# Performance work log

Hardware: AMD Instinct MI355X
Metric: run time of the kernel (lower is better)

Reference implementation:

```python
import jax, jax.numpy as jnp
import numpy as np


def conv1x1(x, w, b):
    # 1x1 Conv2d: x [B,C,H,W], w [O,C], b [O] -> [B,O,H,W]
    return jnp.einsum('bchw,oc->bohw', x, w) + b[None, :, None, None]


def setup_inputs() -> dict:
    key = jax.random.key(0)
    ks = jax.random.split(key, 10)
    B, C, Ci, H, W = 4, 64, 32, 64, 64
    s = 0.05
    return {
        'supp_feature': jax.random.normal(ks[0], (B, C, H, W), jnp.float32),
        'ref_feature': jax.random.normal(ks[1], (B, C, H, W), jnp.float32),
        'theta_w': jax.random.normal(ks[2], (Ci, C), jnp.float32) * s,
        'theta_b': jax.random.normal(ks[3], (Ci,), jnp.float32) * s,
        'phi_w': jax.random.normal(ks[4], (Ci, C), jnp.float32) * s,
        'phi_b': jax.random.normal(ks[5], (Ci,), jnp.float32) * s,
        'g_w': jax.random.normal(ks[6], (Ci, C), jnp.float32) * s,
        'g_b': jax.random.normal(ks[7], (Ci,), jnp.float32) * s,
        'w_w': jax.random.normal(ks[8], (C, Ci), jnp.float32) * s,
        'w_b': jax.random.normal(ks[9], (C,), jnp.float32) * s,
    }


def reference(supp_feature, ref_feature, theta_w, theta_b, phi_w, phi_b,
              g_w, g_b, w_w, w_b):
    B, C, H, W = supp_feature.shape
    Ci = theta_w.shape[0]
    N = H * W
    theta_x = conv1x1(supp_feature, theta_w, theta_b).reshape(B, Ci, N)  # [B,Ci,N]
    phi_y = conv1x1(ref_feature, phi_w, phi_b).reshape(B, Ci, N)        # [B,Ci,M]
    g_y = conv1x1(ref_feature, g_w, g_b).reshape(B, Ci, N)              # [B,Ci,M]
    # f[b,n,m] = <theta_x[b,:,n], phi_y[b,:,m]>  (unscaled)
    f = jnp.einsum('bcn,bcm->bnm', theta_x, phi_y)
    # NOTE: softmax over dim=1 (the QUERY axis n), matching F.softmax(f, dim=1)
    f_div_C = jax.nn.softmax(f, axis=1)
    # x1[b,c,n] = sum_m f_div_C[b,n,m] * g_y[b,c,m]
    x1 = jnp.einsum('bnm,bcm->bcn', f_div_C, g_y).reshape(B, Ci, H, W)
    z = supp_feature + conv1x1(x1, w_w, w_b)
    return z
```

## Files before the change

### kernel.cpp

```cpp
#include <hip/hip_runtime.h>

#define C_ 64
#define CI_ 32
#define N_ 4096
#define LOG2E 1.4426950408889634f

typedef __attribute__((ext_vector_type(8))) short bf16x8;
typedef __attribute__((ext_vector_type(4))) float f32x4;

__device__ __forceinline__ unsigned short f2bf_rne(float f) {
  unsigned u = __builtin_bit_cast(unsigned, f);
  unsigned r = (u + 0x7FFFu + ((u >> 16) & 1u)) >> 16;
  return (unsigned short)r;
}
__device__ __forceinline__ unsigned pack_bf2(float lo, float hi) {
  unsigned a = (__builtin_bit_cast(unsigned, lo) + 0x8000u) >> 16;
  unsigned b = (__builtin_bit_cast(unsigned, hi) + 0x8000u) & 0xFFFF0000u;
  return a | b;
}
__device__ __forceinline__ void dma16(const void* gp, const void* lp) {
  __builtin_amdgcn_global_load_lds(
      (const __attribute__((address_space(1))) unsigned*)(unsigned long long)gp,
      (__attribute__((address_space(3))) unsigned*)(unsigned)(unsigned long long)lp,
      16, 0, 0);
}


__global__ __launch_bounds__(256) void k1_proj(
    const float* __restrict__ supp, const float* __restrict__ ref,
    const float* __restrict__ tw, const float* __restrict__ tb,
    const float* __restrict__ pw, const float* __restrict__ pb,
    const float* __restrict__ gw, const float* __restrict__ gb,
    unsigned short* __restrict__ theta, unsigned short* __restrict__ phi2,
    unsigned short* __restrict__ g2)
{
  const int proj = blockIdx.x >> 8;
  const int rr = blockIdx.x & 255;
  const int b = rr >> 6;
  const int n0 = (rr & 63) << 6;
  const int o = __builtin_amdgcn_readfirstlane(threadIdx.x >> 6);
  const int lane = threadIdx.x & 63;
  const int n = n0 + lane;

  __shared__ float gL[CI_][66];

  const float *W, *bias, *src;
  if (proj == 0)      { W = tw; bias = tb; src = supp; }
  else if (proj == 1) { W = pw; bias = pb; src = ref; }
  else                { W = gw; bias = gb; src = ref; }

  const float* x = src + (size_t)b * (C_ * N_) + n;
  const float* Wo = W + o * 8 * C_;
  float acc[8];
#pragma unroll
  for (int k = 0; k < 8; k++) acc[k] = bias[o * 8 + k];
#pragma unroll 8
  for (int c = 0; c < C_; c++) {
    float v = x[(size_t)c * N_];
#pragma unroll
    for (int k = 0; k < 8; k++) acc[k] = fmaf(Wo[k * C_ + c], v, acc[k]);
  }

  if (proj == 0) {
    unsigned pk[4];
#pragma unroll
    for (int k = 0; k < 4; k++)
      pk[k] = (unsigned)f2bf_rne(acc[2 * k] * LOG2E) |
              ((unsigned)f2bf_rne(acc[2 * k + 1] * LOG2E) << 16);
    *(uint4*)(theta + (((size_t)b * N_ + n) << 5) + o * 8) = *(uint4*)pk;
  } else if (proj == 1) {
    unsigned pk[4];
#pragma unroll
    for (int k = 0; k < 4; k++)
      pk[k] = (unsigned)f2bf_rne(acc[2 * k]) |
              ((unsigned)f2bf_rne(acc[2 * k + 1]) << 16);
    size_t off = (((size_t)b * 128 + (n >> 5)) << 10) + o * 256 + (n & 31) * 8;
    *(uint4*)(phi2 + off) = *(uint4*)pk;
  } else {
#pragma unroll
    for (int k = 0; k < 8; k++) gL[o * 8 + k][lane] = acc[k];
    __syncthreads();
    const int t = threadIdx.x;
    const int c = t >> 7;
    const int rr2 = t & 127;
    const int q = rr2 >> 5;
    const int i = rr2 & 31;
    const float* g0 = &gL[i][c * 32 + 4 * q];
    unsigned pk[4];
    pk[0] = pack_bf2(g0[0], g0[1]);
    pk[1] = pack_bf2(g0[2], g0[3]);
    pk[2] = pack_bf2(g0[16], g0[17]);
    pk[3] = pack_bf2(g0[18], g0[19]);
    size_t off = (((size_t)b * 128 + (n0 >> 5) + c) << 10) + rr2 * 8;
    *(uint4*)(g2 + off) = *(uint4*)pk;
  }
}

__global__ __launch_bounds__(256) void k2_den(
    const unsigned short* __restrict__ theta, const unsigned short* __restrict__ phi2,
    const float* __restrict__ ww, float* __restrict__ den,
    unsigned short* __restrict__ ww2)
{
  const int mt = blockIdx.x & 63;
  const int nq = (blockIdx.x >> 6) & 3;
  const int b = blockIdx.x >> 8;
  const int tid = threadIdx.x;
  const int w = tid >> 6;
  const int lane = tid & 63;
  const int row16 = lane & 15;
  const int quad = lane >> 4;

  if (blockIdx.x == 0) {
    for (int e = tid; e < C_ * CI_; e += 256) {
      int p = e & 31;
      int i = 4 * ((p >> 3) & 3) + (p & 3) + 16 * ((p >> 2) & 1);
      ww2[e] = f2bf_rne(ww[(e >> 5) * CI_ + i]);
    }
  }

  __shared__ __align__(16) unsigned short TH[2][2048];

  bf16x8 bf = *(const bf16x8*)(phi2 +
      (((size_t)b * 128 + mt * 2 + (w >> 1)) << 10) + (quad << 8) +
      ((w & 1) * 16 + row16) * 8);

  const unsigned short* thbase = theta + (((size_t)b * N_ + nq * 1024) << 5);

  dma16(thbase + w * 512 + lane * 8, &TH[0][w * 512]);
  __syncthreads();

  f32x4 zero = {0.f, 0.f, 0.f, 0.f};
  float ds4[4] = {0.f, 0.f, 0.f, 0.f};

  for (int ph = 0; ph < 16; ph++) {
    const int buf = ph & 1;
    if (ph + 1 < 16)
      dma16(thbase + (ph + 1) * 2048 + w * 512 + lane * 8, &TH[buf ^ 1][w * 512]);
#pragma unroll
    for (int s = 0; s < 4; s++) {
      bf16x8 af = *(const bf16x8*)(&TH[buf][s * 512 + row16 * 32 + quad * 8]);
      f32x4 ff = __builtin_amdgcn_mfma_f32_16x16x32_bf16(af, bf, zero, 0, 0, 0);
#pragma unroll
      for (int r = 0; r < 4; r++) ds4[r] += __builtin_amdgcn_exp2f(ff[r]);
    }
    __syncthreads();
  }

  float v = (ds4[0] + ds4[1]) + (ds4[2] + ds4[3]);
  v += __shfl_xor(v, 16);
  v += __shfl_xor(v, 32);
  if (lane < 16) {
    int ml64 = w * 16 + lane;
    int ch = mt * 2 + (ml64 >> 5);
    int local = ml64 & 31;
    int q = (local & 15) >> 2;
    int j = (local & 3) | (((local >> 4) & 1) << 2);
    atomicAdd(&den[(((size_t)b * 128 + ch) << 5) + 8 * q + j], v);
  }
}

__global__ __launch_bounds__(1024) void k3_attn(
    const unsigned short* __restrict__ theta, const unsigned short* __restrict__ phi2,
    const unsigned short* __restrict__ g2, const float* __restrict__ den,
    const unsigned short* __restrict__ ww2, const float* __restrict__ wb,
    const float* __restrict__ supp, float* __restrict__ out)
{
  const int tid = threadIdx.x;
  const int w = tid >> 6;
  const int lane = tid & 63;
  const int b = blockIdx.x >> 6;
  const int n0 = (blockIdx.x & 63) << 6;
  const int ns = w & 3;
  const int q = w >> 2;
  const int row16 = lane & 15;
  const int quad = lane >> 4;

  __shared__ __align__(16) unsigned short SB[2][4][4096];
  __shared__ float rdenL[4096];

  for (int e = tid; e < 4096; e += 1024)
    rdenL[e] = __builtin_amdgcn_rcpf(den[((size_t)b << 12) + e]);

  bf16x8 tB = *(const bf16x8*)(theta +
      (((size_t)b * N_ + n0 + ns * 16 + row16) << 5) + (quad << 3));

  const size_t chb = (size_t)b * 128;
  const int sq = w >> 2;

  f32x4 zero = {0.f, 0.f, 0.f, 0.f};
  f32x4 xa = zero, xb = zero;

#pragma unroll
  for (int s = 0; s < 2; s++) {
    int idx = w * 2 + s;
    int cc = (idx >> 2) & 1;
    int part = idx & 3;
    const unsigned short* src = (part >= 2 ? g2 : phi2) +
        ((chb + sq * 32 + cc) << 10) + ((size_t)(part & 1) << 9) + lane * 8;
    dma16(src, &SB[0][sq][cc * 2048 + (part >= 2 ? 1024 : 0) + ((part & 1) << 9)]);
  }
  __syncthreads();

  for (int ph = 0; ph < 16; ph++) {
    const int buf = ph & 1;
    if (ph + 1 < 16) {
#pragma unroll
      for (int s = 0; s < 2; s++) {
        int idx = w * 2 + s;
        int cc = (idx >> 2) & 1;
        int part = idx & 3;
        const unsigned short* src = (part >= 2 ? g2 : phi2) +
            ((chb + sq * 32 + (ph + 1) * 2 + cc) << 10) + ((size_t)(part & 1) << 9) + lane * 8;
        dma16(src, &SB[buf ^ 1][sq][cc * 2048 + (part >= 2 ? 1024 : 0) + ((part & 1) << 9)]);
      }
    }
#pragma unroll
    for (int cc = 0; cc < 2; cc++) {
      const unsigned short* base = &SB[buf][q][cc * 2048];
      bf16x8 pA0 = *(const bf16x8*)(base + (quad << 8) + row16 * 8);
      bf16x8 pA1 = *(const bf16x8*)(base + (quad << 8) + (row16 + 16) * 8);
      bf16x8 gA0 = *(const bf16x8*)(base + 1024 + (quad << 8) + row16 * 8);
      bf16x8 gA1 = *(const bf16x8*)(base + 1024 + (quad << 8) + (row16 + 16) * 8);
      const float* rp = &rdenL[((q * 32 + ph * 2 + cc) << 5) + (quad << 3)];
      f32x4 r0 = *(const f32x4*)rp;
      f32x4 r1 = *(const f32x4*)(rp + 4);

      f32x4 f0 = __builtin_amdgcn_mfma_f32_16x16x32_bf16(pA0, tB, zero, 0, 0, 0);
      f32x4 f1 = __builtin_amdgcn_mfma_f32_16x16x32_bf16(pA1, tB, zero, 0, 0, 0);

      uint4 d;
      d.x = pack_bf2(__builtin_amdgcn_exp2f(f0[0]) * r0[0],
                     __builtin_amdgcn_exp2f(f0[1]) * r0[1]);
      d.y = pack_bf2(__builtin_amdgcn_exp2f(f0[2]) * r0[2],
                     __builtin_amdgcn_exp2f(f0[3]) * r0[3]);
      d.z = pack_bf2(__builtin_amdgcn_exp2f(f1[0]) * r1[0],
                     __builtin_amdgcn_exp2f(f1[1]) * r1[1]);
      d.w = pack_bf2(__builtin_amdgcn_exp2f(f1[2]) * r1[2],
                     __builtin_amdgcn_exp2f(f1[3]) * r1[3]);
      bf16x8 Pb = __builtin_bit_cast(bf16x8, d);

      xa = __builtin_amdgcn_mfma_f32_16x16x32_bf16(gA0, Pb, xa, 0, 0, 0);
      xb = __builtin_amdgcn_mfma_f32_16x16x32_bf16(gA1, Pb, xb, 0, 0, 0);
    }
    __syncthreads();
  }

  float* part = (float*)SB;
  if (q) {
    float* dst = part + ((((q - 1) * 4 + ns) * 64 + lane) << 3);
#pragma unroll
    for (int r = 0; r < 4; r++) { dst[r] = xa[r]; dst[4 + r] = xb[r]; }
  }
  __syncthreads();
  if (q == 0) {
#pragma unroll
    for (int e = 0; e < 3; e++) {
      const float* s = part + (((e * 4 + ns) * 64 + lane) << 3);
#pragma unroll
      for (int r = 0; r < 4; r++) { xa[r] += s[r]; xb[r] += s[4 + r]; }
    }
    uint4 d;
    d.x = pack_bf2(xa[0], xa[1]);
    d.y = pack_bf2(xa[2], xa[3]);
    d.z = pack_bf2(xb[0], xb[1]);
    d.w = pack_bf2(xb[2], xb[3]);
    bf16x8 Bx = __builtin_bit_cast(bf16x8, d);
    const int nloc = n0 + ns * 16 + row16;
#pragma unroll
    for (int ct = 0; ct < 4; ct++) {
      bf16x8 aw = *(const bf16x8*)(ww2 + (ct * 16 + row16) * CI_ + (quad << 3));
      f32x4 o = __builtin_amdgcn_mfma_f32_16x16x32_bf16(aw, Bx, zero, 0, 0, 0);
#pragma unroll
      for (int r = 0; r < 4; r++) {
        int c = ct * 16 + quad * 4 + r;
        size_t ob = ((size_t)b * C_ + c) * N_ + nloc;
        out[ob] = o[r] + wb[c] + supp[ob];
      }
    }
  }
}

extern "C" void kernel_launch(void* const* d_in, const int* in_sizes, int n_in,
                              void* d_out, int out_size, void* d_ws, size_t ws_size,
                              hipStream_t stream)
{
  const float* supp = (const float*)d_in[0];
  const float* ref  = (const float*)d_in[1];
  const float* tw   = (const float*)d_in[2];
  const float* tb   = (const float*)d_in[3];
  const float* pw   = (const float*)d_in[4];
  const float* pb   = (const float*)d_in[5];
  const float* gw   = (const float*)d_in[6];
  const float* gb   = (const float*)d_in[7];
  const float* ww   = (const float*)d_in[8];
  const float* wb   = (const float*)d_in[9];
  float* out = (float*)d_out;

  char* ws = (char*)d_ws;
  unsigned short* theta = (unsigned short*)ws;
  unsigned short* phi2  = (unsigned short*)(ws + (1u << 20));
  unsigned short* g2    = (unsigned short*)(ws + (2u << 20));
  float*          den   = (float*)(ws + (3u << 20));
  unsigned short* ww2   = (unsigned short*)(ws + (3u << 20) + 65536);

  hipMemsetAsync(den, 0, 4 * 128 * 32 * sizeof(float), stream);
  hipLaunchKernelGGL(k1_proj, dim3(768), dim3(256), 0, stream,
                     supp, ref, tw, tb, pw, pb, gw, gb, theta, phi2, g2);
  hipLaunchKernelGGL(k2_den, dim3(1024), dim3(256), 0, stream,
                     theta, phi2, ww, den, ww2);
  hipLaunchKernelGGL(k3_attn, dim3(256), dim3(1024), 0, stream,
                     theta, phi2, g2, den, ww2, wb, supp, out);
}
```

Before: 114.6 us.

## Fuse three kernels into one persistent kernel with grid-wide barriers

Merges the projection, softmax-denominator and attention kernels into a single 256-block launch of 1024 threads that separates the phases with atomic-counter grid barriers. This removes two kernel launches and their gaps. The reciprocal-denominator multiply is replaced by adding -log2(den) into the MFMA accumulator before exp2, which saves per-element multiplies. The cost is that each phase now runs with fewer blocks and a different work split, and the spin barrier relies on all 256 blocks being resident at once, with a break-out timeout that could let a phase proceed before the others finish.

New measurement: 254.9 us. +122.4%, slower.

```diff
diff --git a/kernel.cpp b/kernel.cpp
--- a/kernel.cpp
+++ b/kernel.cpp
@@ -4,6 +4,7 @@
 #define CI_ 32
 #define N_ 4096
 #define LOG2E 1.4426950408889634f
+#define NBLK 256
 
 typedef __attribute__((ext_vector_type(8))) short bf16x8;
 typedef __attribute__((ext_vector_type(4))) float f32x4;
@@ -25,256 +26,259 @@
       16, 0, 0);
 }
 
-
-__global__ __launch_bounds__(256) void k1_proj(
+__device__ __forceinline__ void grid_sync(unsigned* bar) {
+  __syncthreads();
+  if (threadIdx.x == 0) {
+    __threadfence();
+    __hip_atomic_fetch_add(bar, 1u, __ATOMIC_RELAXED, __HIP_MEMORY_SCOPE_AGENT);
+    unsigned spins = 0;
+    while (__hip_atomic_load(bar, __ATOMIC_RELAXED, __HIP_MEMORY_SCOPE_AGENT) < NBLK) {
+      __builtin_amdgcn_s_sleep(16);
+      if (++spins > 1000000u) break;
+    }
+    __threadfence();
+  }
+  __syncthreads();
+}
+
+__global__ __launch_bounds__(1024) void fused(
     const float* __restrict__ supp, const float* __restrict__ ref,
     const float* __restrict__ tw, const float* __restrict__ tb,
     const float* __restrict__ pw, const float* __restrict__ pb,
     const float* __restrict__ gw, const float* __restrict__ gb,
+    const float* __restrict__ ww, const float* __restrict__ wb,
     unsigned short* __restrict__ theta, unsigned short* __restrict__ phi2,
-    unsigned short* __restrict__ g2)
+    unsigned short* __restrict__ g2, float* __restrict__ den,
+    unsigned short* __restrict__ ww2, unsigned* __restrict__ bar,
+    float* __restrict__ out)
 {
-  const int proj = blockIdx.x >> 8;
-  const int rr = blockIdx.x & 255;
-  const int b = rr >> 6;
-  const int n0 = (rr & 63) << 6;
-  const int o = __builtin_amdgcn_readfirstlane(threadIdx.x >> 6);
-  const int lane = threadIdx.x & 63;
-  const int n = n0 + lane;
-
-  __shared__ float gL[CI_][66];
-
-  const float *W, *bias, *src;
-  if (proj == 0)      { W = tw; bias = tb; src = supp; }
-  else if (proj == 1) { W = pw; bias = pb; src = ref; }
-  else                { W = gw; bias = gb; src = ref; }
-
-  const float* x = src + (size_t)b * (C_ * N_) + n;
-  const float* Wo = W + o * 8 * C_;
-  float acc[8];
-#pragma unroll
-  for (int k = 0; k < 8; k++) acc[k] = bias[o * 8 + k];
-#pragma unroll 8
-  for (int c = 0; c < C_; c++) {
-    float v = x[(size_t)c * N_];
-#pragma unroll
-    for (int k = 0; k < 8; k++) acc[k] = fmaf(Wo[k * C_ + c], v, acc[k]);
-  }
-
-  if (proj == 0) {
-    unsigned pk[4];
-#pragma unroll
-    for (int k = 0; k < 4; k++)
-      pk[k] = (unsigned)f2bf_rne(acc[2 * k] * LOG2E) |
-              ((unsigned)f2bf_rne(acc[2 * k + 1] * LOG2E) << 16);
-    *(uint4*)(theta + (((size_t)b * N_ + n) << 5) + o * 8) = *(uint4*)pk;
-  } else if (proj == 1) {
-    unsigned pk[4];
-#pragma unroll
-    for (int k = 0; k < 4; k++)
-      pk[k] = (unsigned)f2bf_rne(acc[2 * k]) |
-              ((unsigned)f2bf_rne(acc[2 * k + 1]) << 16);
-    size_t off = (((size_t)b * 128 + (n >> 5)) << 10) + o * 256 + (n & 31) * 8;
-    *(uint4*)(phi2 + off) = *(uint4*)pk;
-  } else {
-#pragma unroll
-    for (int k = 0; k < 8; k++) gL[o * 8 + k][lane] = acc[k];
-    __syncthreads();
-    const int t = threadIdx.x;
-    const int c = t >> 7;
-    const int rr2 = t & 127;
-    const int q = rr2 >> 5;
-    const int i = rr2 & 31;
-    const float* g0 = &gL[i][c * 32 + 4 * q];
-    unsigned pk[4];
-    pk[0] = pack_bf2(g0[0], g0[1]);
-    pk[1] = pack_bf2(g0[2], g0[3]);
-    pk[2] = pack_bf2(g0[16], g0[17]);
-    pk[3] = pack_bf2(g0[18], g0[19]);
-    size_t off = (((size_t)b * 128 + (n0 >> 5) + c) << 10) + rr2 * 8;
-    *(uint4*)(g2 + off) = *(uint4*)pk;
-  }
-}
-
-__global__ __launch_bounds__(256) void k2_den(
-    const unsigned short* __restrict__ theta, const unsigned short* __restrict__ phi2,
-    const float* __restrict__ ww, float* __restrict__ den,
-    unsigned short* __restrict__ ww2)
-{
-  const int mt = blockIdx.x & 63;
-  const int nq = (blockIdx.x >> 6) & 3;
-  const int b = blockIdx.x >> 8;
+  __shared__ __align__(16) unsigned char LB[98304];
   const int tid = threadIdx.x;
+  const int bid = blockIdx.x;
+  const int lane = tid & 63;
   const int w = tid >> 6;
-  const int lane = tid & 63;
   const int row16 = lane & 15;
   const int quad = lane >> 4;
 
-  if (blockIdx.x == 0) {
-    for (int e = tid; e < C_ * CI_; e += 256) {
-      int p = e & 31;
-      int i = 4 * ((p >> 3) & 3) + (p & 3) + 16 * ((p >> 2) & 1);
-      ww2[e] = f2bf_rne(ww[(e >> 5) * CI_ + i]);
+  {
+    const int b = bid >> 6;
+    const int n0 = (bid & 63) << 6;
+    const int g = tid >> 8;
+    const int o = __builtin_amdgcn_readfirstlane(w & 3);
+    const int n = n0 + lane;
+    float (*gL)[66] = (float (*)[66])LB;
+
+    if (g < 3) {
+      const float *W, *bias, *src;
+      if (g == 0)      { W = tw; bias = tb; src = supp; }
+      else if (g == 1) { W = pw; bias = pb; src = ref; }
+      else             { W = gw; bias = gb; src = ref; }
+      const float* x = src + (size_t)b * (C_ * N_) + n;
+      const float* Wo = W + o * 8 * C_;
+      float acc[8];
+#pragma unroll
+      for (int k = 0; k < 8; k++) acc[k] = bias[o * 8 + k];
+#pragma unroll 8
+      for (int c = 0; c < C_; c++) {
+        float v = x[(size_t)c * N_];
+#pragma unroll
+        for (int k = 0; k < 8; k++) acc[k] = fmaf(Wo[k * C_ + c], v, acc[k]);
+      }
+      if (g == 0) {
+        unsigned pk[4];
+#pragma unroll
+        for (int k = 0; k < 4; k++)
+          pk[k] = (unsigned)f2bf_rne(acc[2 * k] * LOG2E) |
+                  ((unsigned)f2bf_rne(acc[2 * k + 1] * LOG2E) << 16);
+        *(uint4*)(theta + (((size_t)b * N_ + n) << 5) + o * 8) = *(uint4*)pk;
+      } else if (g == 1) {
+        unsigned pk[4];
+#pragma unroll
+        for (int k = 0; k < 4; k++)
+          pk[k] = (unsigned)f2bf_rne(acc[2 * k]) |
+                  ((unsigned)f2bf_rne(acc[2 * k + 1]) << 16);
+        size_t off = (((size_t)b * 128 + (n >> 5)) << 10) + o * 256 + (n & 31) * 8;
+        *(uint4*)(phi2 + off) = *(uint4*)pk;
+      } else {
+#pragma unroll
+        for (int k = 0; k < 8; k++) gL[o * 8 + k][lane] = acc[k];
+      }
+    } else {
+      if (bid == 16) {
+        for (int e = tid & 255; e < C_ * CI_; e += 256) {
+          int p = e & 31;
+          int i = 4 * ((p >> 3) & 3) + (p & 3) + 16 * ((p >> 2) & 1);
+          ww2[e] = f2bf_rne(ww[(e >> 5) * CI_ + i]);
+        }
+      }
+    }
+    __syncthreads();
+    if (g == 2) {
+      const int t = tid & 255;
+      const int c = t >> 7;
+      const int rr2 = t & 127;
+      const int q = rr2 >> 5;
+      const int i = rr2 & 31;
+      const float* g0 = &gL[i][c * 32 + 4 * q];
+      unsigned pk[4];
+      pk[0] = pack_bf2(g0[0], g0[1]);
+      pk[1] = pack_bf2(g0[2], g0[3]);
+      pk[2] = pack_bf2(g0[16], g0[17]);
+      pk[3] = pack_bf2(g0[18], g0[19]);
+      size_t off = (((size_t)b * 128 + (n0 >> 5) + c) << 10) + rr2 * 8;
+      *(uint4*)(g2 + off) = *(uint4*)pk;
     }
   }
 
-  __shared__ __align__(16) unsigned short TH[2][2048];
-
-  bf16x8 bf = *(const bf16x8*)(phi2 +
-      (((size_t)b * 128 + mt * 2 + (w >> 1)) << 10) + (quad << 8) +
-      ((w & 1) * 16 + row16) * 8);
-
-  const unsigned short* thbase = theta + (((size_t)b * N_ + nq * 1024) << 5);
-
-  dma16(thbase + w * 512 + lane * 8, &TH[0][w * 512]);
-  __syncthreads();
-
-  f32x4 zero = {0.f, 0.f, 0.f, 0.f};
-  float ds4[4] = {0.f, 0.f, 0.f, 0.f};
-
-  for (int ph = 0; ph < 16; ph++) {
-    const int buf = ph & 1;
-    if (ph + 1 < 16)
-      dma16(thbase + (ph + 1) * 2048 + w * 512 + lane * 8, &TH[buf ^ 1][w * 512]);
-#pragma unroll
-    for (int s = 0; s < 4; s++) {
-      bf16x8 af = *(const bf16x8*)(&TH[buf][s * 512 + row16 * 32 + quad * 8]);
-      f32x4 ff = __builtin_amdgcn_mfma_f32_16x16x32_bf16(af, bf, zero, 0, 0, 0);
-#pragma unroll
-      for (int r = 0; r < 4; r++) ds4[r] += __builtin_amdgcn_exp2f(ff[r]);
-    }
+  grid_sync(&bar[0]);
+
+  {
+    const int b = bid >> 6;
+    const int nq = (bid >> 4) & 3;
+    const int mt4 = bid & 15;
+    unsigned short (*TH)[2048] = (unsigned short (*)[2048])LB;
+
+    const int m256 = w * 16 + row16;
+    bf16x8 bf = *(const bf16x8*)(phi2 +
+        (((size_t)b * 128 + mt4 * 8 + (m256 >> 5)) << 10) + (quad << 8) +
+        (m256 & 31) * 8);
+
+    const unsigned short* thbase = theta + (((size_t)b * N_ + nq * 1024) << 5);
+    if (w < 4) dma16(thbase + w * 512 + lane * 8, &TH[0][w * 512]);
     __syncthreads();
+
+    f32x4 zero = {0.f, 0.f, 0.f, 0.f};
+    float ds4[4] = {0.f, 0.f, 0.f, 0.f};
+    for (int ph = 0; ph < 16; ph++) {
+      const int buf = ph & 1;
+      if (ph + 1 < 16 && w < 4)
+        dma16(thbase + (ph + 1) * 2048 + w * 512 + lane * 8, &TH[buf ^ 1][w * 512]);
+#pragma unroll
+      for (int s = 0; s < 4; s++) {
+        bf16x8 af = *(const bf16x8*)(&TH[buf][s * 512 + row16 * 32 + quad * 8]);
+        f32x4 ff = __builtin_amdgcn_mfma_f32_16x16x32_bf16(af, bf, zero, 0, 0, 0);
+#pragma unroll
+        for (int r = 0; r < 4; r++) ds4[r] += __builtin_amdgcn_exp2f(ff[r]);
+      }
+      __syncthreads();
+    }
+    float v = (ds4[0] + ds4[1]) + (ds4[2] + ds4[3]);
+    v += __shfl_xor(v, 16);
+    v += __shfl_xor(v, 32);
+    if (lane < 16) {
+      int ml = w * 16 + lane;
+      int ch = mt4 * 8 + (ml >> 5);
+      int local = ml & 31;
+      int q = (local & 15) >> 2;
+      int j = (local & 3) | (((local >> 4) & 1) << 2);
+      atomicAdd(&den[(((size_t)b * 128 + ch) << 5) + 8 * q + j], v);
+    }
   }
 
-  float v = (ds4[0] + ds4[1]) + (ds4[2] + ds4[3]);
-  v += __shfl_xor(v, 16);
-  v += __shfl_xor(v, 32);
-  if (lane < 16) {
-    int ml64 = w * 16 + lane;
-    int ch = mt * 2 + (ml64 >> 5);
-    int local = ml64 & 31;
-    int q = (local & 15) >> 2;
-    int j = (local & 3) | (((local >> 4) & 1) << 2);
-    atomicAdd(&den[(((size_t)b * 128 + ch) << 5) + 8 * q + j], v);
-  }
-}
-
-__global__ __launch_bounds__(1024) void k3_attn(
-    const unsigned short* __restrict__ theta, const unsigned short* __restrict__ phi2,
-    const unsigned short* __restrict__ g2, const float* __restrict__ den,
-    const unsigned short* __restrict__ ww2, const float* __restrict__ wb,
-    const float* __restrict__ supp, float* __restrict__ out)
-{
-  const int tid = threadIdx.x;
-  const int w = tid >> 6;
-  const int lane = tid & 63;
-  const int b = blockIdx.x >> 6;
-  const int n0 = (blockIdx.x & 63) << 6;
-  const int ns = w & 3;
-  const int q = w >> 2;
-  const int row16 = lane & 15;
-  const int quad = lane >> 4;
-
-  __shared__ __align__(16) unsigned short SB[2][4][4096];
-  __shared__ float rdenL[4096];
-
-  for (int e = tid; e < 4096; e += 1024)
-    rdenL[e] = __builtin_amdgcn_rcpf(den[((size_t)b << 12) + e]);
-
-  bf16x8 tB = *(const bf16x8*)(theta +
-      (((size_t)b * N_ + n0 + ns * 16 + row16) << 5) + (quad << 3));
-
-  const size_t chb = (size_t)b * 128;
-  const int sq = w >> 2;
-
-  f32x4 zero = {0.f, 0.f, 0.f, 0.f};
-  f32x4 xa = zero, xb = zero;
-
-#pragma unroll
-  for (int s = 0; s < 2; s++) {
-    int idx = w * 2 + s;
-    int cc = (idx >> 2) & 1;
-    int part = idx & 3;
-    const unsigned short* src = (part >= 2 ? g2 : phi2) +
-        ((chb + sq * 32 + cc) << 10) + ((size_t)(part & 1) << 9) + lane * 8;
-    dma16(src, &SB[0][sq][cc * 2048 + (part >= 2 ? 1024 : 0) + ((part & 1) << 9)]);
-  }
-  __syncthreads();
-
-  for (int ph = 0; ph < 16; ph++) {
-    const int buf = ph & 1;
-    if (ph + 1 < 16) {
-#pragma unroll
-      for (int s = 0; s < 2; s++) {
-        int idx = w * 2 + s;
-        int cc = (idx >> 2) & 1;
-        int part = idx & 3;
-        const unsigned short* src = (part >= 2 ? g2 : phi2) +
-            ((chb + sq * 32 + (ph + 1) * 2 + cc) << 10) + ((size_t)(part & 1) << 9) + lane * 8;
-        dma16(src, &SB[buf ^ 1][sq][cc * 2048 + (part >= 2 ? 1024 : 0) + ((part & 1) << 9)]);
-      }
-    }
-#pragma unroll
-    for (int cc = 0; cc < 2; cc++) {
-      const unsigned short* base = &SB[buf][q][cc * 2048];
-      bf16x8 pA0 = *(const bf16x8*)(base + (quad << 8) + row16 * 8);
-      bf16x8 pA1 = *(const bf16x8*)(base + (quad << 8) + (row16 + 16) * 8);
-      bf16x8 gA0 = *(const bf16x8*)(base + 1024 + (quad << 8) + row16 * 8);
-      bf16x8 gA1 = *(const bf16x8*)(base + 1024 + (quad << 8) + (row16 + 16) * 8);
-      const float* rp = &rdenL[((q * 32 + ph * 2 + cc) << 5) + (quad << 3)];
-      f32x4 r0 = *(const f32x4*)rp;
-      f32x4 r1 = *(const f32x4*)(rp + 4);
-
-      f32x4 f0 = __builtin_amdgcn_mfma_f32_16x16x32_bf16(pA0, tB, zero, 0, 0, 0);
-      f32x4 f1 = __builtin_amdgcn_mfma_f32_16x16x32_bf16(pA1, tB, zero, 0, 0, 0);
-
+  grid_sync(&bar[1]);
+
+  {
+    const int b = bid >> 6;
+    const int n0 = (bid & 63) << 6;
+    const int ns = w & 3;
+    const int q = w >> 2;
+    unsigned short (*SB)[4][4096] = (unsigned short (*)[4][4096])LB;
+    float* ldL = (float*)(LB + 65536);
+
+    for (int e = tid; e < 4096; e += 1024)
+      ldL[e] = -__log2f(den[((size_t)b << 12) + e]);
+
+    bf16x8 tB = *(const bf16x8*)(theta +
+        (((size_t)b * N_ + n0 + ns * 16 + row16) << 5) + (quad << 3));
+
+    const size_t chb = (size_t)b * 128;
+    const int sq = w >> 2;
+
+    f32x4 zero = {0.f, 0.f, 0.f, 0.f};
+    f32x4 xa = zero, xb = zero;
+
+#pragma unroll
+    for (int s = 0; s < 2; s++) {
+      int idx = w * 2 + s;
+      int cc = (idx >> 2) & 1;
+      int part = idx & 3;
+      const unsigned short* src = (part >= 2 ? g2 : phi2) +
+          ((chb + sq * 32 + cc) << 10) + ((size_t)(part & 1) << 9) + lane * 8;
+      dma16(src, &SB[0][sq][cc * 2048 + (part >= 2 ? 1024 : 0) + ((part & 1) << 9)]);
+    }
+    __syncthreads();
+
+    for (int ph = 0; ph < 16; ph++) {
+      const int buf = ph & 1;
+      if (ph + 1 < 16) {
+#pragma unroll
+        for (int s = 0; s < 2; s++) {
+          int idx = w * 2 + s;
+          int cc = (idx >> 2) & 1;
+          int part = idx & 3;
+          const unsigned short* src = (part >= 2 ? g2 : phi2) +
+              ((chb + sq * 32 + (ph + 1) * 2 + cc) << 10) + ((size_t)(part & 1) << 9) + lane * 8;
+          dma16(src, &SB[buf ^ 1][sq][cc * 2048 + (part >= 2 ? 1024 : 0) + ((part & 1) << 9)]);
+        }
+      }
+#pragma unroll
+      for (int cc = 0; cc < 2; cc++) {
+        const unsigned short* base = &SB[buf][q][cc * 2048];
+        bf16x8 pA0 = *(const bf16x8*)(base + (quad << 8) + row16 * 8);
+        bf16x8 pA1 = *(const bf16x8*)(base + (quad << 8) + (row16 + 16) * 8);
+        bf16x8 gA0 = *(const bf16x8*)(base + 1024 + (quad << 8) + row16 * 8);
+        bf16x8 gA1 = *(const bf16x8*)(base + 1024 + (quad << 8) + (row16 + 16) * 8);
+        const float* lp = &ldL[((q * 32 + ph * 2 + cc) << 5) + (quad << 3)];
+        f32x4 l0 = *(const f32x4*)lp;
+        f32x4 l1 = *(const f32x4*)(lp + 4);
+
+        f32x4 f0 = __builtin_amdgcn_mfma_f32_16x16x32_bf16(pA0, tB, l0, 0, 0, 0);
+        f32x4 f1 = __builtin_amdgcn_mfma_f32_16x16x32_bf16(pA1, tB, l1, 0, 0, 0);
+
+        uint4 d;
+        d.x = pack_bf2(__builtin_amdgcn_exp2f(f0[0]), __builtin_amdgcn_exp2f(f0[1]));
+        d.y = pack_bf2(__builtin_amdgcn_exp2f(f0[2]), __builtin_amdgcn_exp2f(f0[3]));
+        d.z = pack_bf2(__builtin_amdgcn_exp2f(f1[0]), __builtin_amdgcn_exp2f(f1[1]));
+        d.w = pack_bf2(__builtin_amdgcn_exp2f(f1[2]), __builtin_amdgcn_exp2f(f1[3]));
+        bf16x8 Pb = __builtin_bit_cast(bf16x8, d);
+
+        xa = __builtin_amdgcn_mfma_f32_16x16x32_bf16(gA0, Pb, xa, 0, 0, 0);
+        xb = __builtin_amdgcn_mfma_f32_16x16x32_bf16(gA1, Pb, xb, 0, 0, 0);
+      }
+      __syncthreads();
+    }
+
+    float* part = (float*)LB;
+    if (q) {
+      float* dst = part + ((((q - 1) * 4 + ns) * 64 + lane) << 3);
+#pragma unroll
+      for (int r = 0; r < 4; r++) { dst[r] = xa[r]; dst[4 + r] = xb[r]; }
+    }
+    __syncthreads();
+    if (q == 0) {
+#pragma unroll
+      for (int e = 0; e < 3; e++) {
+        const float* s = part + (((e * 4 + ns) * 64 + lane) << 3);
+#pragma unroll
+        for (int r = 0; r < 4; r++) { xa[r] += s[r]; xb[r] += s[4 + r]; }
+      }
       uint4 d;
-      d.x = pack_bf2(__builtin_amdgcn_exp2f(f0[0]) * r0[0],
-                     __builtin_amdgcn_exp2f(f0[1]) * r0[1]);
-      d.y = pack_bf2(__builtin_amdgcn_exp2f(f0[2]) * r0[2],
-                     __builtin_amdgcn_exp2f(f0[3]) * r0[3]);
-      d.z = pack_bf2(__builtin_amdgcn_exp2f(f1[0]) * r1[0],
-                     __builtin_amdgcn_exp2f(f1[1]) * r1[1]);
-      d.w = pack_bf2(__builtin_amdgcn_exp2f(f1[2]) * r1[2],
-                     __builtin_amdgcn_exp2f(f1[3]) * r1[3]);
-      bf16x8 Pb = __builtin_bit_cast(bf16x8, d);
-
-      xa = __builtin_amdgcn_mfma_f32_16x16x32_bf16(gA0, Pb, xa, 0, 0, 0);
-      xb = __builtin_amdgcn_mfma_f32_16x16x32_bf16(gA1, Pb, xb, 0, 0, 0);
-    }
-    __syncthreads();
-  }
-
-  float* part = (float*)SB;
-  if (q) {
-    float* dst = part + ((((q - 1) * 4 + ns) * 64 + lane) << 3);
-#pragma unroll
-    for (int r = 0; r < 4; r++) { dst[r] = xa[r]; dst[4 + r] = xb[r]; }
-  }
-  __syncthreads();
-  if (q == 0) {
-#pragma unroll
-    for (int e = 0; e < 3; e++) {
-      const float* s = part + (((e * 4 + ns) * 64 + lane) << 3);
-#pragma unroll
-      for (int r = 0; r < 4; r++) { xa[r] += s[r]; xb[r] += s[4 + r]; }
-    }
-    uint4 d;
-    d.x = pack_bf2(xa[0], xa[1]);
-    d.y = pack_bf2(xa[2], xa[3]);
-    d.z = pack_bf2(xb[0], xb[1]);
-    d.w = pack_bf2(xb[2], xb[3]);
-    bf16x8 Bx = __builtin_bit_cast(bf16x8, d);
-    const int nloc = n0 + ns * 16 + row16;
-#pragma unroll
-    for (int ct = 0; ct < 4; ct++) {
-      bf16x8 aw = *(const bf16x8*)(ww2 + (ct * 16 + row16) * CI_ + (quad << 3));
-      f32x4 o = __builtin_amdgcn_mfma_f32_16x16x32_bf16(aw, Bx, zero, 0, 0, 0);
-#pragma unroll
-      for (int r = 0; r < 4; r++) {
-        int c = ct * 16 + quad * 4 + r;
-        size_t ob = ((size_t)b * C_ + c) * N_ + nloc;
-        out[ob] = o[r] + wb[c] + supp[ob];
+      d.x = pack_bf2(xa[0], xa[1]);
+      d.y = pack_bf2(xa[2], xa[3]);
+      d.z = pack_bf2(xb[0], xb[1]);
+      d.w = pack_bf2(xb[2], xb[3]);
+      bf16x8 Bx = __builtin_bit_cast(bf16x8, d);
+      const int nloc = n0 + ns * 16 + row16;
+#pragma unroll
+      for (int ct = 0; ct < 4; ct++) {
+        bf16x8 aw = *(const bf16x8*)(ww2 + (ct * 16 + row16) * CI_ + (quad << 3));
+        f32x4 o = __builtin_amdgcn_mfma_f32_16x16x32_bf16(aw, Bx, zero, 0, 0, 0);
+#pragma unroll
+        for (int r = 0; r < 4; r++) {
+          int c = ct * 16 + quad * 4 + r;
+          size_t ob = ((size_t)b * C_ + c) * N_ + nloc;
+          out[ob] = o[r] + wb[c] + supp[ob];
+        }
       }
     }
   }
@@ -302,12 +306,10 @@
   unsigned short* g2    = (unsigned short*)(ws + (2u << 20));
   float*          den   = (float*)(ws + (3u << 20));
   unsigned short* ww2   = (unsigned short*)(ws + (3u << 20) + 65536);
-
-  hipMemsetAsync(den, 0, 4 * 128 * 32 * sizeof(float), stream);
-  hipLaunchKernelGGL(k1_proj, dim3(768), dim3(256), 0, stream,
-                     supp, ref, tw, tb, pw, pb, gw, gb, theta, phi2, g2);
-  hipLaunchKernelGGL(k2_den, dim3(1024), dim3(256), 0, stream,
-                     theta, phi2, ww, den, ww2);
-  hipLaunchKernelGGL(k3_attn, dim3(256), dim3(1024), 0, stream,
-                     theta, phi2, g2, den, ww2, wb, supp, out);
-}
+  unsigned*       bar   = (unsigned*)(ws + (3u << 20) + 65536 + 4096);
+
+  hipMemsetAsync(ws + (3u << 20), 0, 65536 + 4096 + 256, stream);
+  hipLaunchKernelGGL(fused, dim3(NBLK), dim3(1024), 0, stream,
+                     supp, ref, tw, tb, pw, pb, gw, gb, ww, wb,
+                     theta, phi2, g2, den, ww2, bar, out);
+}
```

## Fold softmax denominator into MFMA accumulator, fuse den zeroing, remap attn blocks

Applied to the files above, without the earlier changes.

Three changes. The softmax normalisation multiply is replaced by adding -log2(den) as the initial accumulator of the score MFMA, so exp2 directly yields normalised probabilities and eight multiplies per step disappear. The separate hipMemsetAsync of the denominator buffer is removed and the zeroing moved into the first 16 blocks of the projection kernel, saving a launch. The attention kernel's block-to-(batch,tile) mapping is interleaved across batches, possibly to spread L2/channel traffic. A per-element log2 replaces the reciprocal in the preload; since the exponent shift is applied before rounding, precision may change slightly.

Measured after the change: 112.8 us (median of 2 runs). About the same (-1.6%).

```diff
diff --git a/kernel.cpp b/kernel.cpp
--- a/kernel.cpp
+++ b/kernel.cpp
@@ -32,7 +32,7 @@
     const float* __restrict__ pw, const float* __restrict__ pb,
     const float* __restrict__ gw, const float* __restrict__ gb,
     unsigned short* __restrict__ theta, unsigned short* __restrict__ phi2,
-    unsigned short* __restrict__ g2)
+    unsigned short* __restrict__ g2, float* __restrict__ den)
 {
   const int proj = blockIdx.x >> 8;
   const int rr = blockIdx.x & 255;
@@ -41,6 +41,11 @@
   const int o = __builtin_amdgcn_readfirstlane(threadIdx.x >> 6);
   const int lane = threadIdx.x & 63;
   const int n = n0 + lane;
+
+  if (blockIdx.x < 16) {
+    uint4 z = {0u, 0u, 0u, 0u};
+    *(uint4*)(den + blockIdx.x * 1024 + threadIdx.x * 4) = z;
+  }
 
   __shared__ float gL[CI_][66];
 
@@ -168,18 +173,20 @@
   const int tid = threadIdx.x;
   const int w = tid >> 6;
   const int lane = tid & 63;
-  const int b = blockIdx.x >> 6;
-  const int n0 = (blockIdx.x & 63) << 6;
+  const int p = blockIdx.x;
+  const int b = (p & 7) >> 1;
+  const int t = ((p >> 3) << 1) | (p & 1);
+  const int n0 = t << 6;
   const int ns = w & 3;
   const int q = w >> 2;
   const int row16 = lane & 15;
   const int quad = lane >> 4;
 
   __shared__ __align__(16) unsigned short SB[2][4][4096];
-  __shared__ float rdenL[4096];
+  __shared__ float ldL[4096];
 
   for (int e = tid; e < 4096; e += 1024)
-    rdenL[e] = __builtin_amdgcn_rcpf(den[((size_t)b << 12) + e]);
+    ldL[e] = -__log2f(den[((size_t)b << 12) + e]);
 
   bf16x8 tB = *(const bf16x8*)(theta +
       (((size_t)b * N_ + n0 + ns * 16 + row16) << 5) + (quad << 3));
@@ -221,22 +228,18 @@
       bf16x8 pA1 = *(const bf16x8*)(base + (quad << 8) + (row16 + 16) * 8);
       bf16x8 gA0 = *(const bf16x8*)(base + 1024 + (quad << 8) + row16 * 8);
       bf16x8 gA1 = *(const bf16x8*)(base + 1024 + (quad << 8) + (row16 + 16) * 8);
-      const float* rp = &rdenL[((q * 32 + ph * 2 + cc) << 5) + (quad << 3)];
-      f32x4 r0 = *(const f32x4*)rp;
-      f32x4 r1 = *(const f32x4*)(rp + 4);
-
-      f32x4 f0 = __builtin_amdgcn_mfma_f32_16x16x32_bf16(pA0, tB, zero, 0, 0, 0);
-      f32x4 f1 = __builtin_amdgcn_mfma_f32_16x16x32_bf16(pA1, tB, zero, 0, 0, 0);
+      const float* lp = &ldL[((q * 32 + ph * 2 + cc) << 5) + (quad << 3)];
+      f32x4 l0 = *(const f32x4*)lp;
+      f32x4 l1 = *(const f32x4*)(lp + 4);
+
+      f32x4 f0 = __builtin_amdgcn_mfma_f32_16x16x32_bf16(pA0, tB, l0, 0, 0, 0);
+      f32x4 f1 = __builtin_amdgcn_mfma_f32_16x16x32_bf16(pA1, tB, l1, 0, 0, 0);
 
       uint4 d;
-      d.x = pack_bf2(__builtin_amdgcn_exp2f(f0[0]) * r0[0],
-                     __builtin_amdgcn_exp2f(f0[1]) * r0[1]);
-      d.y = pack_bf2(__builtin_amdgcn_exp2f(f0[2]) * r0[2],
-                     __builtin_amdgcn_exp2f(f0[3]) * r0[3]);
-      d.z = pack_bf2(__builtin_amdgcn_exp2f(f1[0]) * r1[0],
-                     __builtin_amdgcn_exp2f(f1[1]) * r1[1]);
-      d.w = pack_bf2(__builtin_amdgcn_exp2f(f1[2]) * r1[2],
-                     __builtin_amdgcn_exp2f(f1[3]) * r1[3]);
+      d.x = pack_bf2(__builtin_amdgcn_exp2f(f0[0]), __builtin_amdgcn_exp2f(f0[1]));
+      d.y = pack_bf2(__builtin_amdgcn_exp2f(f0[2]), __builtin_amdgcn_exp2f(f0[3]));
+      d.z = pack_bf2(__builtin_amdgcn_exp2f(f1[0]), __builtin_amdgcn_exp2f(f1[1]));
+      d.w = pack_bf2(__builtin_amdgcn_exp2f(f1[2]), __builtin_amdgcn_exp2f(f1[3]));
       bf16x8 Pb = __builtin_bit_cast(bf16x8, d);
 
       xa = __builtin_amdgcn_mfma_f32_16x16x32_bf16(gA0, Pb, xa, 0, 0, 0);
@@ -303,9 +306,8 @@
   float*          den   = (float*)(ws + (3u << 20));
   unsigned short* ww2   = (unsigned short*)(ws + (3u << 20) + 65536);
 
-  hipMemsetAsync(den, 0, 4 * 128 * 32 * sizeof(float), stream);
   hipLaunchKernelGGL(k1_proj, dim3(768), dim3(256), 0, stream,
-                     supp, ref, tw, tb, pw, pb, gw, gb, theta, phi2, g2);
+                     supp, ref, tw, tb, pw, pb, gw, gb, theta, phi2, g2, den);
   hipLaunchKernelGGL(k2_den, dim3(1024), dim3(256), 0, stream,
                      theta, phi2, ww, den, ww2);
   hipLaunchKernelGGL(k3_attn, dim3(256), dim3(1024), 0, stream,
```
